# Kernel tuning notes

Hardware: AMD Instinct MI355X
Metric: run time of the kernel (lower is better)

Reference implementation:

```python
import jax, jax.numpy as jnp
import numpy as np

BETA = 0.25

def setup_inputs() -> dict:
    key = jax.random.key(0)
    k1, k2 = jax.random.split(key)
    x = jax.random.normal(k1, (16, 32, 32, 256), dtype=jnp.float32)
    embed = jax.random.normal(k2, (256, 8192), dtype=jnp.float32)
    return {"x": x, "embed": embed}

def reference(x, embed):
    dim = embed.shape[0]
    flatten = x.reshape(-1, dim)  # [N, dim]
    # squared L2 distance to each code: ||f||^2 - 2 f.e + ||e||^2 -> [N, n_embed]
    dist = (jnp.sum(flatten * flatten, axis=1, keepdims=True)
            - 2.0 * (flatten @ embed)
            + jnp.sum(embed * embed, axis=0, keepdims=True))
    ind = jnp.argmin(dist, axis=1)  # == argmax(-dist)
    embed_ind = ind.reshape(x.shape[:-1])  # [B, H, W]
    codebook = embed.T  # [n_embed, dim]
    quantize = codebook[embed_ind]  # gather -> [B, H, W, dim]
    diff = jnp.mean((jax.lax.stop_gradient(quantize) - x) ** 2)
    commit_loss = jnp.mean((quantize - jax.lax.stop_gradient(x)) ** 2)
    diff = diff + commit_loss * BETA
    quantize = x + jax.lax.stop_gradient(quantize - x)  # straight-through
    return quantize, diff, embed_ind
```

## Files before the change

kernel.cpp:

```cpp
#include <hip/hip_runtime.h>

static constexpr int DIM   = 256;
static constexpr int NCODE = 8192;
static constexpr int NROWS = 16384;

typedef __bf16 bf16x8 __attribute__((ext_vector_type(8)));
typedef float  f32x4  __attribute__((ext_vector_type(4)));

__device__ __forceinline__ void gload_lds16(const void* g, void* l) {
    __builtin_amdgcn_global_load_lds(
        (const __attribute__((address_space(1))) void*)g,
        (__attribute__((address_space(3))) void*)l, 16, 0, 0);
}

__device__ __forceinline__ void top2_insert(float& v0, int& i0, float& v1, int& i1,
                                            float s, int si) {
    if (s < v0) { v1 = v0; i1 = i0; v0 = s; i0 = si; }
    else if (s < v1) { v1 = s; i1 = si; }
}
__device__ __forceinline__ void top2_merge(float& v0, int& i0, float& v1, int& i1,
                                           float b0, int bi0, float b1, int bi1) {
    if (b0 < v0) {
        if (b1 < v0) { v0 = b0; i0 = bi0; v1 = b1; i1 = bi1; }
        else         { v1 = v0; i1 = i0;  v0 = b0; i0 = bi0; }
    } else if (b0 < v1) { v1 = b0; i1 = bi0; }
}

__global__ __launch_bounds__(256) void cvt_x_kernel(const float* __restrict__ x,
                                                    ushort* __restrict__ xb) {
    int i = blockIdx.x * 256 + threadIdx.x;
    const float4* xp = (const float4*)x + (size_t)i * 2;
    float4 a = xp[0], b = xp[1];
    bf16x8 o;
    o[0] = (__bf16)a.x; o[1] = (__bf16)a.y; o[2] = (__bf16)a.z; o[3] = (__bf16)a.w;
    o[4] = (__bf16)b.x; o[5] = (__bf16)b.y; o[6] = (__bf16)b.z; o[7] = (__bf16)b.w;
    ((bf16x8*)xb)[i] = o;
}

__global__ __launch_bounds__(256) void cvt_e_kernel(const float* __restrict__ embed,
                                                    ushort* __restrict__ eb16,
                                                    float* __restrict__ ebT32) {
    __shared__ float tile[64][65];
    const int c00 = blockIdx.x * 64;
    const int k0  = blockIdx.y * 64;
    const int t   = threadIdx.x;
    const int tc  = t & 63, tr4 = t >> 6;
    #pragma unroll
    for (int i = 0; i < 16; ++i) {
        int r = i * 4 + tr4;
        tile[r][tc] = embed[(size_t)(k0 + r) * NCODE + c00 + tc];
    }
    __syncthreads();
    const int cl = t >> 2;
    const int kq = t & 3;
    float vals[16];
    #pragma unroll
    for (int j = 0; j < 16; ++j) vals[j] = tile[kq * 16 + j][cl];
    float* d32 = ebT32 + (size_t)(c00 + cl) * DIM + k0 + kq * 16;
    #pragma unroll
    for (int j = 0; j < 4; ++j)
        *(float4*)(d32 + j * 4) = make_float4(vals[j*4], vals[j*4+1], vals[j*4+2], vals[j*4+3]);
    bf16x8 h0, h1;
    #pragma unroll
    for (int j = 0; j < 8; ++j) { h0[j] = (__bf16)vals[j]; h1[j] = (__bf16)vals[8 + j]; }
    ushort* d16 = eb16 + (size_t)(c00 + cl) * DIM + k0 + kq * 16;
    *(bf16x8*)d16 = h0;
    *(bf16x8*)(d16 + 8) = h1;
}

__global__ __launch_bounds__(256) void e2_kernel(const float* __restrict__ embed,
                                                 float* __restrict__ e2) {
    int j = blockIdx.x * 256 + threadIdx.x;
    float s = 0.f;
    for (int k = 0; k < DIM; ++k) {
        float v = embed[(size_t)k * NCODE + j];
        s = __fadd_rn(s, __fmul_rn(v, v));
    }
    e2[j] = s;
}

__global__ __launch_bounds__(256) void gemm_top2_kernel(
    const ushort* __restrict__ xb,
    const ushort* __restrict__ eb,
    const float* __restrict__ e2,
    uint4* __restrict__ scratch)
{
    __shared__ ushort As[2][4096];
    __shared__ ushort Bs[2][4096];

    const int t    = threadIdx.x;
    const int c0   = blockIdx.x * 128;
    const int r0   = blockIdx.y * 128;
    const int wid  = t >> 6, lane = t & 63;
    const int wr   = wid >> 1, wc = wid & 1;
    const int lr   = lane & 15, g = lane >> 4;

    auto stage = [&](int buf, int ks) {
        #pragma unroll
        for (int i = 0; i < 2; ++i) {
            int o   = t * 16 + i * 4096;
            int row = o >> 6;
            int s   = (o >> 4) & 3;
            gload_lds16(xb + (size_t)(r0 + row) * DIM + ks * 32 + s * 8, &As[buf][o >> 1]);
        }
        #pragma unroll
        for (int i = 0; i < 2; ++i) {
            int o   = t * 16 + i * 4096;
            int row = o >> 6;
            int s   = (o >> 4) & 3;
            gload_lds16(eb + (size_t)(c0 + row) * DIM + ks * 32 + s * 8, &Bs[buf][o >> 1]);
        }
    };

    f32x4 acc[4][4];
    #pragma unroll
    for (int a = 0; a < 4; ++a)
        #pragma unroll
        for (int b = 0; b < 4; ++b) acc[a][b] = (f32x4){0.f, 0.f, 0.f, 0.f};

    stage(0, 0);
    int cur = 0;
    for (int ks = 0; ks < 8; ++ks) {
        __syncthreads();
        if (ks < 7) stage(cur ^ 1, ks + 1);
        bf16x8 af[4], bfr[4];
        const char* Ab = (const char*)&As[cur][0];
        const char* Bb = (const char*)&Bs[cur][0];
        #pragma unroll
        for (int fr = 0; fr < 4; ++fr) {
            int row = wr * 64 + fr * 16 + lr;
            af[fr] = *(const bf16x8*)(Ab + row * 64 + g * 16);
        }
        #pragma unroll
        for (int fc = 0; fc < 4; ++fc) {
            int code = wc * 64 + fc * 16 + lr;
            bfr[fc] = *(const bf16x8*)(Bb + code * 64 + g * 16);
        }
        #pragma unroll
        for (int fr = 0; fr < 4; ++fr)
            #pragma unroll
            for (int fc = 0; fc < 4; ++fc)
                acc[fr][fc] = __builtin_amdgcn_mfma_f32_16x16x32_bf16(
                    af[fr], bfr[fc], acc[fr][fc], 0, 0, 0);
        cur ^= 1;
    }

    __syncthreads();
    uint4* ldsT = (uint4*)&As[0][0];

    float e2v[4];
    #pragma unroll
    for (int fc = 0; fc < 4; ++fc) e2v[fc] = e2[c0 + wc * 64 + fc * 16 + lr];

    #pragma unroll
    for (int fr = 0; fr < 4; ++fr) {
        #pragma unroll
        for (int reg = 0; reg < 4; ++reg) {
            float v0 = __builtin_inff(), v1 = __builtin_inff();
            int   i0 = -1, i1 = -1;
            #pragma unroll
            for (int fc = 0; fc < 4; ++fc) {
                float sv = __builtin_fmaf(-2.f, acc[fr][fc][reg], e2v[fc]);
                top2_insert(v0, i0, v1, i1, sv, c0 + wc * 64 + fc * 16 + lr);
            }
            #pragma unroll
            for (int m = 1; m < 16; m <<= 1) {
                float b0 = __shfl_xor(v0, m), b1 = __shfl_xor(v1, m);
                int  bi0 = __shfl_xor(i0, m), bi1 = __shfl_xor(i1, m);
                top2_merge(v0, i0, v1, i1, b0, bi0, b1, bi1);
            }
            if (lr == 0)
                ldsT[wid * 64 + fr * 16 + g * 4 + reg] =
                    make_uint4(__float_as_uint(v0), (unsigned)i0,
                               __float_as_uint(v1), (unsigned)i1);
        }
    }
    __syncthreads();
    if (t < 128) {
        int wrh = t >> 6, rl = t & 63;
        uint4 A = ldsT[(wrh * 2 + 0) * 64 + rl];
        uint4 B = ldsT[(wrh * 2 + 1) * 64 + rl];
        float v0 = __uint_as_float(A.x), v1 = __uint_as_float(A.z);
        int   i0 = (int)A.y,             i1 = (int)A.w;
        top2_merge(v0, i0, v1, i1, __uint_as_float(B.x), (int)B.y,
                   __uint_as_float(B.z), (int)B.w);
        scratch[(size_t)(r0 + t) * 64 + blockIdx.x] =
            make_uint4(__float_as_uint(v0), (unsigned)i0,
                       __float_as_uint(v1), (unsigned)i1);
    }
}

__global__ __launch_bounds__(256) void band_kernel(
    const uint4* __restrict__ scratch,
    unsigned* __restrict__ lists, unsigned* __restrict__ counts)
{
    const int row  = blockIdx.x * 4 + (threadIdx.x >> 6);
    const int lane = threadIdx.x & 63;
    uint4 e = scratch[(size_t)row * 64 + lane];
    float v0 = __uint_as_float(e.x), v1 = __uint_as_float(e.z);
    float m = v0;
    #pragma unroll
    for (int s = 1; s < 64; s <<= 1) m = fminf(m, __shfl_xor(m, s));
    const float thr = m + 1.0f;
    bool f0 = v0 <= thr, f1 = v1 <= thr;
    unsigned long long b0 = __ballot(f0);
    unsigned long long b1 = __ballot(f1);
    int c0 = __popcll(b0);
    int p0 = __popcll(b0 & ((1ull << lane) - 1));
    int p1 = c0 + __popcll(b1 & ((1ull << lane) - 1));
    if (f0 && p0 < 16) lists[(size_t)row * 16 + p0] = e.y;
    if (f1 && p1 < 16) lists[(size_t)row * 16 + p1] = e.w;
    if (lane == 0) counts[row] = (unsigned)min(c0 + __popcll(b1), 16);
}

__global__ __launch_bounds__(256) void rescore_kernel(
    const float* __restrict__ x, const float* __restrict__ ebT32,
    const float* __restrict__ e2, const unsigned* __restrict__ lists,
    const unsigned* __restrict__ counts, unsigned* __restrict__ best_idx)
{
    const int t    = threadIdx.x;
    const int row  = blockIdx.x * 16 + (t >> 4);
    const int slot = t & 15;
    const int cnt  = (int)counts[row];
    float d = __builtin_inff();
    unsigned idx = 0xFFFFFFFFu;
    if (slot < cnt) {
        idx = lists[(size_t)row * 16 + slot];
        const float* xr = x + (size_t)row * DIM;
        const float* er = ebT32 + (size_t)idx * DIM;
        float f2 = 0.f, dot = 0.f;
        for (int k = 0; k < DIM; ++k) {
            float xv = xr[k];
            f2  = __fadd_rn(f2, __fmul_rn(xv, xv));
            dot = __builtin_fmaf(xv, er[k], dot);
        }
        d = __fadd_rn(__builtin_fmaf(-2.f, dot, f2), e2[idx]);
    }
    #pragma unroll
    for (int m = 1; m < 16; m <<= 1) {
        float    od = __shfl_xor(d, m);
        unsigned oi = (unsigned)__shfl_xor((int)idx, m);
        if (od < d || (od == d && oi < idx)) { d = od; idx = oi; }
    }
    if (slot == 0) best_idx[row] = idx;
}

__global__ __launch_bounds__(256) void output_kernel(
    const float* __restrict__ x, const float* __restrict__ ebT32,
    const unsigned* __restrict__ best_idx,
    float* __restrict__ quant, float* __restrict__ diff, float* __restrict__ ind)
{
    const int row = blockIdx.x;
    const int d   = threadIdx.x;
    const unsigned idx = best_idx[row];

    float xv = x[(size_t)row * DIM + d];
    float q  = ebT32[(size_t)idx * DIM + d];
    float dq = __fsub_rn(q, xv);
    quant[(size_t)row * DIM + d] = __fadd_rn(xv, dq);

    float c = __fmul_rn(dq, dq);
    #pragma unroll
    for (int off = 32; off >= 1; off >>= 1) c += __shfl_down(c, off);

    __shared__ float partial[4];
    if ((d & 63) == 0) partial[d >> 6] = c;
    __syncthreads();
    if (d == 0) {
        float s = (partial[0] + partial[1]) + (partial[2] + partial[3]);
        atomicAdd(diff, s * (1.25f / 4194304.f));
        ind[row] = (float)idx;
    }
}

extern "C" void kernel_launch(void* const* d_in, const int* in_sizes, int n_in,
                              void* d_out, int out_size, void* d_ws, size_t ws_size,
                              hipStream_t stream)
{
    const float* x     = (const float*)d_in[0];
    const float* embed = (const float*)d_in[1];

    float* out   = (float*)d_out;
    float* quant = out;
    float* diff  = out + 4194304;
    float* ind   = out + 4194305;

    char* w = (char*)d_ws;
    ushort*   xb      = (ushort*)(w);
    ushort*   eb16    = (ushort*)(w + 8388608);
    float*    ebT32   = (float*) (w + 12582912);
    float*    e2      = (float*) (w + 20971520);
    unsigned* lists   = (unsigned*)(w + 21004288);
    unsigned* counts  = (unsigned*)(w + 22052864);
    unsigned* bestidx = (unsigned*)(w + 22118400);

    uint4* scratch = (uint4*)quant;

    cvt_x_kernel<<<2048, 256, 0, stream>>>(x, xb);
    cvt_e_kernel<<<dim3(128, 4), 256, 0, stream>>>(embed, eb16, ebT32);
    e2_kernel<<<32, 256, 0, stream>>>(embed, e2);
    gemm_top2_kernel<<<dim3(64, 128), 256, 0, stream>>>(xb, eb16, e2, scratch);
    band_kernel<<<4096, 256, 0, stream>>>(scratch, lists, counts);
    rescore_kernel<<<1024, 256, 0, stream>>>(x, ebT32, e2, lists, counts, bestidx);
    hipMemsetAsync(diff, 0, sizeof(float), stream);
    output_kernel<<<NROWS, 256, 0, stream>>>(x, ebT32, bestidx, quant, diff, ind);
}
```

Measured before the change: 752.1 us.

## Fuse prep kernels, restructure GEMM with full-K LDS tile, fuse band+rescore

Merges the three preprocessing kernels into one launch. The GEMM now uses 512 threads and loads the entire K=256 slab of A and B into XOR-swizzled LDS in one pass instead of double-buffering 32-wide K slices, with a block-index swizzle for L2 locality. The band selection and rescore are fused into one kernel that passes candidates through LDS, removing the lists/counts global round trip. The trade-off is 128KB LDS per block, which limits the GEMM to one block per CU with no load/compute overlap.

```diff
diff --git a/kernel.cpp b/kernel.cpp
--- a/kernel.cpp
+++ b/kernel.cpp
@@ -26,131 +26,139 @@
     } else if (b0 < v1) { v1 = b0; i1 = bi0; }
 }
 
-__global__ __launch_bounds__(256) void cvt_x_kernel(const float* __restrict__ x,
-                                                    ushort* __restrict__ xb) {
-    int i = blockIdx.x * 256 + threadIdx.x;
-    const float4* xp = (const float4*)x + (size_t)i * 2;
-    float4 a = xp[0], b = xp[1];
-    bf16x8 o;
-    o[0] = (__bf16)a.x; o[1] = (__bf16)a.y; o[2] = (__bf16)a.z; o[3] = (__bf16)a.w;
-    o[4] = (__bf16)b.x; o[5] = (__bf16)b.y; o[6] = (__bf16)b.z; o[7] = (__bf16)b.w;
-    ((bf16x8*)xb)[i] = o;
-}
-
-__global__ __launch_bounds__(256) void cvt_e_kernel(const float* __restrict__ embed,
-                                                    ushort* __restrict__ eb16,
-                                                    float* __restrict__ ebT32) {
+__global__ __launch_bounds__(256) void prep_kernel(
+    const float* __restrict__ x, const float* __restrict__ embed,
+    ushort* __restrict__ xb, ushort* __restrict__ eb16,
+    float* __restrict__ ebT32, float* __restrict__ e2)
+{
     __shared__ float tile[64][65];
-    const int c00 = blockIdx.x * 64;
-    const int k0  = blockIdx.y * 64;
-    const int t   = threadIdx.x;
-    const int tc  = t & 63, tr4 = t >> 6;
-    #pragma unroll
-    for (int i = 0; i < 16; ++i) {
-        int r = i * 4 + tr4;
-        tile[r][tc] = embed[(size_t)(k0 + r) * NCODE + c00 + tc];
-    }
-    __syncthreads();
-    const int cl = t >> 2;
-    const int kq = t & 3;
-    float vals[16];
-    #pragma unroll
-    for (int j = 0; j < 16; ++j) vals[j] = tile[kq * 16 + j][cl];
-    float* d32 = ebT32 + (size_t)(c00 + cl) * DIM + k0 + kq * 16;
-    #pragma unroll
-    for (int j = 0; j < 4; ++j)
-        *(float4*)(d32 + j * 4) = make_float4(vals[j*4], vals[j*4+1], vals[j*4+2], vals[j*4+3]);
-    bf16x8 h0, h1;
-    #pragma unroll
-    for (int j = 0; j < 8; ++j) { h0[j] = (__bf16)vals[j]; h1[j] = (__bf16)vals[8 + j]; }
-    ushort* d16 = eb16 + (size_t)(c00 + cl) * DIM + k0 + kq * 16;
-    *(bf16x8*)d16 = h0;
-    *(bf16x8*)(d16 + 8) = h1;
-}
-
-__global__ __launch_bounds__(256) void e2_kernel(const float* __restrict__ embed,
-                                                 float* __restrict__ e2) {
-    int j = blockIdx.x * 256 + threadIdx.x;
-    float s = 0.f;
-    for (int k = 0; k < DIM; ++k) {
-        float v = embed[(size_t)k * NCODE + j];
-        s = __fadd_rn(s, __fmul_rn(v, v));
-    }
-    e2[j] = s;
-}
-
-__global__ __launch_bounds__(256) void gemm_top2_kernel(
+    const int b = blockIdx.x;
+    const int t = threadIdx.x;
+
+    if (b < 2048) {
+        int i = b * 256 + t;
+        const float4* xp = (const float4*)x + (size_t)i * 2;
+        float4 a = xp[0], v = xp[1];
+        bf16x8 o;
+        o[0] = (__bf16)a.x; o[1] = (__bf16)a.y; o[2] = (__bf16)a.z; o[3] = (__bf16)a.w;
+        o[4] = (__bf16)v.x; o[5] = (__bf16)v.y; o[6] = (__bf16)v.z; o[7] = (__bf16)v.w;
+        ((bf16x8*)xb)[i] = o;
+    } else if (b < 2560) {
+        const int eb = b - 2048;
+        const int c00 = (eb & 127) * 64;
+        const int k0  = (eb >> 7) * 64;
+        const int tc  = t & 63, tr4 = t >> 6;
+        #pragma unroll
+        for (int i = 0; i < 16; ++i) {
+            int r = i * 4 + tr4;
+            tile[r][tc] = embed[(size_t)(k0 + r) * NCODE + c00 + tc];
+        }
+        __syncthreads();
+        const int cl = t >> 2;
+        const int kq = t & 3;
+        float vals[16];
+        #pragma unroll
+        for (int j = 0; j < 16; ++j) vals[j] = tile[kq * 16 + j][cl];
+        float* d32 = ebT32 + (size_t)(c00 + cl) * DIM + k0 + kq * 16;
+        #pragma unroll
+        for (int j = 0; j < 4; ++j)
+            *(float4*)(d32 + j * 4) = make_float4(vals[j*4], vals[j*4+1],
+                                                  vals[j*4+2], vals[j*4+3]);
+        bf16x8 h0, h1;
+        #pragma unroll
+        for (int j = 0; j < 8; ++j) { h0[j] = (__bf16)vals[j]; h1[j] = (__bf16)vals[8 + j]; }
+        ushort* d16 = eb16 + (size_t)(c00 + cl) * DIM + k0 + kq * 16;
+        *(bf16x8*)d16 = h0;
+        *(bf16x8*)(d16 + 8) = h1;
+    } else {
+        int j = (b - 2560) * 256 + t;
+        float s = 0.f;
+        for (int k = 0; k < DIM; ++k) {
+            float v = embed[(size_t)k * NCODE + j];
+            s = __fadd_rn(s, __fmul_rn(v, v));
+        }
+        e2[j] = s;
+    }
+}
+
+__global__ __launch_bounds__(512, 1) void gemm_top2_kernel(
     const ushort* __restrict__ xb,
     const ushort* __restrict__ eb,
     const float* __restrict__ e2,
     uint4* __restrict__ scratch)
 {
-    __shared__ ushort As[2][4096];
-    __shared__ ushort Bs[2][4096];
-
-    const int t    = threadIdx.x;
-    const int c0   = blockIdx.x * 128;
-    const int r0   = blockIdx.y * 128;
-    const int wid  = t >> 6, lane = t & 63;
-    const int wr   = wid >> 1, wc = wid & 1;
-    const int lr   = lane & 15, g = lane >> 4;
-
-    auto stage = [&](int buf, int ks) {
-        #pragma unroll
-        for (int i = 0; i < 2; ++i) {
-            int o   = t * 16 + i * 4096;
-            int row = o >> 6;
-            int s   = (o >> 4) & 3;
-            gload_lds16(xb + (size_t)(r0 + row) * DIM + ks * 32 + s * 8, &As[buf][o >> 1]);
-        }
-        #pragma unroll
-        for (int i = 0; i < 2; ++i) {
-            int o   = t * 16 + i * 4096;
-            int row = o >> 6;
-            int s   = (o >> 4) & 3;
-            gload_lds16(eb + (size_t)(c0 + row) * DIM + ks * 32 + s * 8, &Bs[buf][o >> 1]);
-        }
-    };
-
-    f32x4 acc[4][4];
+    __shared__ ushort As[32768];
+    __shared__ ushort Bs[32768];
+
+    const int t = threadIdx.x;
+
+    const int lin   = blockIdx.y * 64 + blockIdx.x;
+    const int swz   = (lin & 7) * 1024 + (lin >> 3);
+    const int chunk = swz & 63;
+    const int rb    = swz >> 6;
+    const int c0    = chunk * 128;
+    const int r0    = rb * 128;
+
+    const ushort* abase = xb + (size_t)r0 * DIM;
+    const ushort* bbase = eb + (size_t)c0 * DIM;
+    #pragma unroll
+    for (int i = 0; i < 8; ++i) {
+        int o   = i * 8192 + t * 16;
+        int row = o >> 9;
+        int cs  = (o & 511) ^ ((row & 7) << 4);
+        gload_lds16(abase + row * DIM + (cs >> 1), &As[o >> 1]);
+    }
+    #pragma unroll
+    for (int i = 0; i < 8; ++i) {
+        int o   = i * 8192 + t * 16;
+        int row = o >> 9;
+        int cs  = (o & 511) ^ ((row & 7) << 4);
+        gload_lds16(bbase + row * DIM + (cs >> 1), &Bs[o >> 1]);
+    }
+    __syncthreads();
+
+    const int wid = t >> 6, lane = t & 63;
+    const int wr  = wid >> 2, wc = wid & 3;
+    const int lr  = lane & 15, g = lane >> 4;
+
+    f32x4 acc[4][2];
     #pragma unroll
     for (int a = 0; a < 4; ++a)
         #pragma unroll
-        for (int b = 0; b < 4; ++b) acc[a][b] = (f32x4){0.f, 0.f, 0.f, 0.f};
-
-    stage(0, 0);
-    int cur = 0;
+        for (int bq = 0; bq < 2; ++bq) acc[a][bq] = (f32x4){0.f, 0.f, 0.f, 0.f};
+
+    const char* Ab = (const char*)As;
+    const char* Bb = (const char*)Bs;
+
+    #pragma unroll
     for (int ks = 0; ks < 8; ++ks) {
-        __syncthreads();
-        if (ks < 7) stage(cur ^ 1, ks + 1);
-        bf16x8 af[4], bfr[4];
-        const char* Ab = (const char*)&As[cur][0];
-        const char* Bb = (const char*)&Bs[cur][0];
+        bf16x8 af[4], bfr[2];
         #pragma unroll
         for (int fr = 0; fr < 4; ++fr) {
             int row = wr * 64 + fr * 16 + lr;
-            af[fr] = *(const bf16x8*)(Ab + row * 64 + g * 16);
-        }
-        #pragma unroll
-        for (int fc = 0; fc < 4; ++fc) {
-            int code = wc * 64 + fc * 16 + lr;
-            bfr[fc] = *(const bf16x8*)(Bb + code * 64 + g * 16);
+            int col = (ks * 64 + g * 16) ^ ((row & 7) << 4);
+            af[fr] = *(const bf16x8*)(Ab + row * 512 + col);
+        }
+        #pragma unroll
+        for (int fc = 0; fc < 2; ++fc) {
+            int code = wc * 32 + fc * 16 + lr;
+            int col  = (ks * 64 + g * 16) ^ ((code & 7) << 4);
+            bfr[fc] = *(const bf16x8*)(Bb + code * 512 + col);
         }
         #pragma unroll
         for (int fr = 0; fr < 4; ++fr)
             #pragma unroll
-            for (int fc = 0; fc < 4; ++fc)
+            for (int fc = 0; fc < 2; ++fc)
                 acc[fr][fc] = __builtin_amdgcn_mfma_f32_16x16x32_bf16(
                     af[fr], bfr[fc], acc[fr][fc], 0, 0, 0);
-        cur ^= 1;
     }
 
     __syncthreads();
-    uint4* ldsT = (uint4*)&As[0][0];
-
-    float e2v[4];
-    #pragma unroll
-    for (int fc = 0; fc < 4; ++fc) e2v[fc] = e2[c0 + wc * 64 + fc * 16 + lr];
+    uint4* ldsM = (uint4*)As;
+
+    float e2v[2];
+    #pragma unroll
+    for (int fc = 0; fc < 2; ++fc) e2v[fc] = e2[c0 + wc * 32 + fc * 16 + lr];
 
     #pragma unroll
     for (int fr = 0; fr < 4; ++fr) {
@@ -159,9 +167,9 @@
             float v0 = __builtin_inff(), v1 = __builtin_inff();
             int   i0 = -1, i1 = -1;
             #pragma unroll
-            for (int fc = 0; fc < 4; ++fc) {
+            for (int fc = 0; fc < 2; ++fc) {
                 float sv = __builtin_fmaf(-2.f, acc[fr][fc][reg], e2v[fc]);
-                top2_insert(v0, i0, v1, i1, sv, c0 + wc * 64 + fc * 16 + lr);
+                top2_insert(v0, i0, v1, i1, sv, c0 + wc * 32 + fc * 16 + lr);
             }
             #pragma unroll
             for (int m = 1; m < 16; m <<= 1) {
@@ -170,7 +178,7 @@
                 top2_merge(v0, i0, v1, i1, b0, bi0, b1, bi1);
             }
             if (lr == 0)
-                ldsT[wid * 64 + fr * 16 + g * 4 + reg] =
+                ldsM[(wr * 4 + wc) * 64 + fr * 16 + g * 4 + reg] =
                     make_uint4(__float_as_uint(v0), (unsigned)i0,
                                __float_as_uint(v1), (unsigned)i1);
         }
@@ -178,24 +186,31 @@
     __syncthreads();
     if (t < 128) {
         int wrh = t >> 6, rl = t & 63;
-        uint4 A = ldsT[(wrh * 2 + 0) * 64 + rl];
-        uint4 B = ldsT[(wrh * 2 + 1) * 64 + rl];
-        float v0 = __uint_as_float(A.x), v1 = __uint_as_float(A.z);
-        int   i0 = (int)A.y,             i1 = (int)A.w;
-        top2_merge(v0, i0, v1, i1, __uint_as_float(B.x), (int)B.y,
-                   __uint_as_float(B.z), (int)B.w);
-        scratch[(size_t)(r0 + t) * 64 + blockIdx.x] =
+        uint4 E = ldsM[(wrh * 4 + 0) * 64 + rl];
+        float v0 = __uint_as_float(E.x), v1 = __uint_as_float(E.z);
+        int   i0 = (int)E.y,             i1 = (int)E.w;
+        #pragma unroll
+        for (int w2 = 1; w2 < 4; ++w2) {
+            uint4 F = ldsM[(wrh * 4 + w2) * 64 + rl];
+            top2_merge(v0, i0, v1, i1, __uint_as_float(F.x), (int)F.y,
+                       __uint_as_float(F.z), (int)F.w);
+        }
+        scratch[(size_t)(r0 + wrh * 64 + rl) * 64 + chunk] =
             make_uint4(__float_as_uint(v0), (unsigned)i0,
                        __float_as_uint(v1), (unsigned)i1);
     }
 }
 
-__global__ __launch_bounds__(256) void band_kernel(
-    const uint4* __restrict__ scratch,
-    unsigned* __restrict__ lists, unsigned* __restrict__ counts)
-{
-    const int row  = blockIdx.x * 4 + (threadIdx.x >> 6);
+__global__ __launch_bounds__(256) void band_rescore_kernel(
+    const uint4* __restrict__ scratch, const float* __restrict__ x,
+    const float* __restrict__ ebT32, const float* __restrict__ e2,
+    unsigned* __restrict__ best_idx)
+{
+    __shared__ unsigned cand[4][16];
+    const int w    = threadIdx.x >> 6;
     const int lane = threadIdx.x & 63;
+    const int row  = blockIdx.x * 4 + w;
+
     uint4 e = scratch[(size_t)row * 64 + lane];
     float v0 = __uint_as_float(e.x), v1 = __uint_as_float(e.z);
     float m = v0;
@@ -205,27 +220,17 @@
     bool f0 = v0 <= thr, f1 = v1 <= thr;
     unsigned long long b0 = __ballot(f0);
     unsigned long long b1 = __ballot(f1);
-    int c0 = __popcll(b0);
-    int p0 = __popcll(b0 & ((1ull << lane) - 1));
-    int p1 = c0 + __popcll(b1 & ((1ull << lane) - 1));
-    if (f0 && p0 < 16) lists[(size_t)row * 16 + p0] = e.y;
-    if (f1 && p1 < 16) lists[(size_t)row * 16 + p1] = e.w;
-    if (lane == 0) counts[row] = (unsigned)min(c0 + __popcll(b1), 16);
-}
-
-__global__ __launch_bounds__(256) void rescore_kernel(
-    const float* __restrict__ x, const float* __restrict__ ebT32,
-    const float* __restrict__ e2, const unsigned* __restrict__ lists,
-    const unsigned* __restrict__ counts, unsigned* __restrict__ best_idx)
-{
-    const int t    = threadIdx.x;
-    const int row  = blockIdx.x * 16 + (t >> 4);
-    const int slot = t & 15;
-    const int cnt  = (int)counts[row];
+    int c0n = __popcll(b0);
+    int p0  = __popcll(b0 & ((1ull << lane) - 1));
+    int p1  = c0n + __popcll(b1 & ((1ull << lane) - 1));
+    if (f0 && p0 < 16) cand[w][p0] = e.y;
+    if (f1 && p1 < 16) cand[w][p1] = e.w;
+    int cnt = min(c0n + __popcll(b1), 16);
+
     float d = __builtin_inff();
     unsigned idx = 0xFFFFFFFFu;
-    if (slot < cnt) {
-        idx = lists[(size_t)row * 16 + slot];
+    if (lane < cnt) {
+        idx = cand[w][lane];
         const float* xr = x + (size_t)row * DIM;
         const float* er = ebT32 + (size_t)idx * DIM;
         float f2 = 0.f, dot = 0.f;
@@ -237,12 +242,12 @@
         d = __fadd_rn(__builtin_fmaf(-2.f, dot, f2), e2[idx]);
     }
     #pragma unroll
-    for (int m = 1; m < 16; m <<= 1) {
-        float    od = __shfl_xor(d, m);
-        unsigned oi = (unsigned)__shfl_xor((int)idx, m);
+    for (int mm = 1; mm < 16; mm <<= 1) {
+        float    od = __shfl_xor(d, mm);
+        unsigned oi = (unsigned)__shfl_xor((int)idx, mm);
         if (od < d || (od == d && oi < idx)) { d = od; idx = oi; }
     }
-    if (slot == 0) best_idx[row] = idx;
+    if (lane == 0) best_idx[row] = idx;
 }
 
 __global__ __launch_bounds__(256) void output_kernel(
@@ -290,18 +295,13 @@
     ushort*   eb16    = (ushort*)(w + 8388608);
     float*    ebT32   = (float*) (w + 12582912);
     float*    e2      = (float*) (w + 20971520);
-    unsigned* lists   = (unsigned*)(w + 21004288);
-    unsigned* counts  = (unsigned*)(w + 22052864);
-    unsigned* bestidx = (unsigned*)(w + 22118400);
+    unsigned* bestidx = (unsigned*)(w + 21004288);
 
     uint4* scratch = (uint4*)quant;
 
-    cvt_x_kernel<<<2048, 256, 0, stream>>>(x, xb);
-    cvt_e_kernel<<<dim3(128, 4), 256, 0, stream>>>(embed, eb16, ebT32);
-    e2_kernel<<<32, 256, 0, stream>>>(embed, e2);
-    gemm_top2_kernel<<<dim3(64, 128), 256, 0, stream>>>(xb, eb16, e2, scratch);
-    band_kernel<<<4096, 256, 0, stream>>>(scratch, lists, counts);
-    rescore_kernel<<<1024, 256, 0, stream>>>(x, ebT32, e2, lists, counts, bestidx);
+    prep_kernel<<<2592, 256, 0, stream>>>(x, embed, xb, eb16, ebT32, e2);
+    gemm_top2_kernel<<<dim3(64, 128), 512, 0, stream>>>(xb, eb16, e2, scratch);
+    band_rescore_kernel<<<4096, 256, 0, stream>>>(scratch, x, ebT32, e2, bestidx);
     hipMemsetAsync(diff, 0, sizeof(float), stream);
     output_kernel<<<NROWS, 256, 0, stream>>>(x, ebT32, bestidx, quant, diff, ind);
 }
```

After: 862.0 us. 14.6% more time.
